# Performance work log

Hardware: AMD Instinct MI355X
Metric: run time of the kernel (lower is better)

## Reference

```python
import jax, jax.numpy as jnp
import numpy as np

H, DH = 16, 64            # heads, dim_head
SCALE = DH ** -0.5
TOPK = 32                  # sparse_topk


def setup_inputs() -> dict:
    key = jax.random.key(0)
    ks = jax.random.split(key, 8)
    b, n, dim = 2, 1024, 1024
    inner = H * DH
    x = jax.random.normal(ks[0], (b, n, dim), jnp.float32)
    rel_pos = jax.random.normal(ks[1], (1, H, n, n), jnp.float32)
    Wq = jax.random.normal(ks[2], (dim, inner), jnp.float32) * 0.02
    Wkv = jax.random.normal(ks[3], (dim, 2 * inner), jnp.float32) * 0.02
    pre_proj = jax.random.normal(ks[4], (H, H), jnp.float32)   # pre_softmax_proj
    post_proj = jax.random.normal(ks[5], (H, H), jnp.float32)  # post_softmax_proj
    Wout = jax.random.normal(ks[6], (inner, dim), jnp.float32) * 0.02
    bout = jnp.zeros((dim,), jnp.float32)
    return dict(x=x, rel_pos=rel_pos, Wq=Wq, Wkv=Wkv, pre_proj=pre_proj,
                post_proj=post_proj, Wout=Wout, bout=bout)


def reference(x, rel_pos, Wq, Wkv, pre_proj, post_proj, Wout, bout):
    b, n, _ = x.shape
    # projections (no bias, matching nn.Linear(..., bias=False))
    q = (x @ Wq).reshape(b, n, H, DH).transpose(0, 2, 1, 3)          # b h n d
    k, v = jnp.split(x @ Wkv, 2, axis=-1)
    k = k.reshape(b, n, H, DH).transpose(0, 2, 1, 3)
    v = v.reshape(b, n, H, DH).transpose(0, 2, 1, 3)
    # scores + rel_pos bias
    dots = jnp.einsum('bhid,bhjd->bhij', q, k) * SCALE + rel_pos
    # talking heads (pre-softmax), applied BEFORE masks as in the source
    dots = jnp.einsum('bhij,hk->bkij', dots, pre_proj)
    neg = -jnp.finfo(dots.dtype).max
    # causal mask
    causal = jnp.triu(jnp.ones((n, n), dtype=bool), 1)
    dots = jnp.where(causal, neg, dots)
    # sparse top-k masking: keep only entries >= k-th largest per row
    kth = jax.lax.top_k(dots, TOPK)[0][..., -1:]
    dots = jnp.where(dots < kth, neg, dots)
    attn = jax.nn.softmax(dots, axis=-1)
    # talking heads (post-softmax)
    attn = jnp.einsum('bhij,hk->bkij', attn, post_proj)
    out = jnp.einsum('bhij,bhjd->bhid', attn, v)
    out = out.transpose(0, 2, 1, 3).reshape(b, n, H * DH)
    return out @ Wout + bout
```

## Files before the change

### kernel.cpp

```cpp
#include <hip/hip_runtime.h>
#include <hip/hip_bf16.h>
#include <float.h>
#include <math.h>

#define HH 16
#define DH 64
#define NS 1024
#define SCALE 0.125f
#define KTOP 32
#define NEGF (-FLT_MAX)

typedef __attribute__((ext_vector_type(8))) short short8;
typedef __attribute__((ext_vector_type(4))) float f32x4;
typedef unsigned short ushort_t;

__device__ __forceinline__ ushort_t f2b(float f) {
    __hip_bfloat16 h = __float2bfloat16(f);
    return *reinterpret_cast<ushort_t*>(&h);
}

__global__ __launch_bounds__(256) void k0_cvt(const float* __restrict__ src,
        ushort_t* __restrict__ dst, int n8) {
    int i = blockIdx.x * 256 + threadIdx.x;
    if (i >= n8) return;
    const float4* s4 = (const float4*)src;
    float4 a = s4[i*2], b = s4[i*2+1];
    short8 o;
    o[0]=f2b(a.x); o[1]=f2b(a.y); o[2]=f2b(a.z); o[3]=f2b(a.w);
    o[4]=f2b(b.x); o[5]=f2b(b.y); o[6]=f2b(b.z); o[7]=f2b(b.w);
    *(short8*)(dst + i*8) = o;
}

__global__ __launch_bounds__(256) void k0_tr(const float* __restrict__ src,
        ushort_t* __restrict__ dst, int N) {
    __shared__ float sh[32][33];
    int tx = threadIdx.x & 31, ty = threadIdx.x >> 5;
    int n0 = blockIdx.x * 32, k0 = blockIdx.y * 32;
    #pragma unroll
    for (int e = 0; e < 4; ++e) {
        int r = ty + e*8;
        sh[r][tx] = src[(k0 + r)*N + n0 + tx];
    }
    __syncthreads();
    #pragma unroll
    for (int e = 0; e < 4; ++e) {
        int r = ty + e*8;
        dst[(n0 + r)*1024 + k0 + tx] = f2b(sh[tx][r]);
    }
}

__global__ __launch_bounds__(256) void k1_mfma(const ushort_t* __restrict__ xb,
        const ushort_t* __restrict__ Wt, ushort_t* __restrict__ qb,
        ushort_t* __restrict__ kbf, ushort_t* __restrict__ vb) {
    __shared__ ushort_t As[128*40];
    __shared__ ushort_t Bs[128*40];
    int t = threadIdx.x;
    int lane = t & 63, w = t >> 6;
    int wm = w >> 1, wn = w & 1;
    int row_l = lane & 15, grp = lane >> 4;
    int row0 = blockIdx.y * 128, col0 = blockIdx.x * 128;
    f32x4 acc[4][4];
    f32x4 zz = {0.f, 0.f, 0.f, 0.f};
    #pragma unroll
    for (int mi = 0; mi < 4; ++mi)
        #pragma unroll
        for (int ni = 0; ni < 4; ++ni) acc[mi][ni] = zz;
    for (int k0 = 0; k0 < 1024; k0 += 32) {
        #pragma unroll
        for (int e = 0; e < 2; ++e) {
            int slot = t + 256*e;
            int r = slot >> 2, kbk = slot & 3;
            short8 vA = *(const short8*)(xb + (row0 + r)*1024 + k0 + kbk*8);
            *(short8*)(As + r*40 + kbk*8) = vA;
            short8 vB = *(const short8*)(Wt + (col0 + r)*1024 + k0 + kbk*8);
            *(short8*)(Bs + r*40 + kbk*8) = vB;
        }
        __syncthreads();
        short8 a[4], b[4];
        #pragma unroll
        for (int mi = 0; mi < 4; ++mi)
            a[mi] = *(const short8*)(As + (wm*64 + mi*16 + row_l)*40 + grp*8);
        #pragma unroll
        for (int ni = 0; ni < 4; ++ni)
            b[ni] = *(const short8*)(Bs + (wn*64 + ni*16 + row_l)*40 + grp*8);
        #pragma unroll
        for (int mi = 0; mi < 4; ++mi)
            #pragma unroll
            for (int ni = 0; ni < 4; ++ni)
                acc[mi][ni] = __builtin_amdgcn_mfma_f32_16x16x32_bf16(
                    a[mi], b[ni], acc[mi][ni], 0, 0, 0);
        __syncthreads();
    }
    #pragma unroll
    for (int mi = 0; mi < 4; ++mi)
        #pragma unroll
        for (int ni = 0; ni < 4; ++ni)
            #pragma unroll
            for (int rg = 0; rg < 4; ++rg) {
                int grow = row0 + wm*64 + mi*16 + grp*4 + rg;
                int gcol = col0 + wn*64 + ni*16 + row_l;
                float val = acc[mi][ni][rg];
                int b_ = grow >> 10, i = grow & 1023;
                int which = gcol >> 10, cc = gcol & 1023;
                int h = cc >> 6, d = cc & 63;
                int idx = (((b_*HH + h)*NS) + i)*DH + d;
                if (which == 0)      qb[idx]  = f2b(val);
                else if (which == 1) kbf[idx] = f2b(val);
                else                 vb[idx]  = f2b(val);
            }
}

__global__ __launch_bounds__(256) void k4_vt(const ushort_t* __restrict__ vb,
        ushort_t* __restrict__ vT) {
    __shared__ ushort_t sh[32][33];
    int bh = blockIdx.z;
    int d0 = blockIdx.x * 32;
    int i0 = blockIdx.y * 32;
    int tx = threadIdx.x & 31, ty = threadIdx.x >> 5;
    #pragma unroll
    for (int e = 0; e < 4; ++e) {
        int r = ty + e*8;
        sh[r][tx] = vb[((size_t)bh*NS + i0 + r)*DH + d0 + tx];
    }
    __syncthreads();
    #pragma unroll
    for (int e = 0; e < 4; ++e) {
        int r = ty + e*8;
        vT[((size_t)bh*DH + d0 + r)*NS + i0 + tx] = sh[tx][r];
    }
}

__global__ __launch_bounds__(256) void k2_scores(const ushort_t* __restrict__ qb,
        const ushort_t* __restrict__ kbf, const float* __restrict__ rel,
        const float* __restrict__ pre, float* __restrict__ dots) {
    int t = threadIdx.x & 63;
    int w = threadIdx.x >> 6;
    int wid = blockIdx.x * 4 + w;
    int b_ = (wid >= 2080) ? 1 : 0;
    int r = wid - 2080*b_;
    int i16 = (int)((sqrtf(8.0f*(float)r + 1.0f) - 1.0f) * 0.5f);
    while ((i16+1)*(i16+2)/2 <= r) ++i16;
    while (i16*(i16+1)/2 > r) --i16;
    int j16 = r - i16*(i16+1)/2;
    int row_l = t & 15, grp = t >> 4;
    int qrow = i16*16 + row_l;
    int krow = j16*16 + row_l;
    int dbase = grp*8;
    float acc[16][4];
    #pragma unroll
    for (int kp = 0; kp < 16; ++kp)
        #pragma unroll
        for (int rg = 0; rg < 4; ++rg) acc[kp][rg] = 0.f;
    #pragma unroll 4
    for (int h = 0; h < HH; ++h) {
        const ushort_t* qh = qb + (((b_*HH + h)*NS) + qrow)*DH;
        const ushort_t* kh = kbf + (((b_*HH + h)*NS) + krow)*DH;
        short8 a0 = *(const short8*)(qh + dbase);
        short8 a1 = *(const short8*)(qh + 32 + dbase);
        short8 b0 = *(const short8*)(kh + dbase);
        short8 b1 = *(const short8*)(kh + 32 + dbase);
        f32x4 s = {0.f, 0.f, 0.f, 0.f};
        s = __builtin_amdgcn_mfma_f32_16x16x32_bf16(a0, b0, s, 0, 0, 0);
        s = __builtin_amdgcn_mfma_f32_16x16x32_bf16(a1, b1, s, 0, 0, 0);
        float pr[16];
        #pragma unroll
        for (int kp = 0; kp < 16; ++kp) pr[kp] = pre[h*16 + kp];
        #pragma unroll
        for (int rg = 0; rg < 4; ++rg) {
            int gi = i16*16 + grp*4 + rg;
            int gj = j16*16 + row_l;
            float tv = s[rg]*SCALE + rel[(h*NS + gi)*NS + gj];
            #pragma unroll
            for (int kp = 0; kp < 16; ++kp) acc[kp][rg] += tv * pr[kp];
        }
    }
    int gj = j16*16 + row_l;
    #pragma unroll
    for (int kp = 0; kp < 16; ++kp)
        #pragma unroll
        for (int rg = 0; rg < 4; ++rg) {
            int gi = i16*16 + grp*4 + rg;
            dots[(((b_*HH + kp)*NS) + gi)*NS + gj] = acc[kp][rg];
        }
}

template<int NC>
__device__ __forceinline__ void topk_row(const float* __restrict__ rowp,
        float* __restrict__ scRow, int i, int l) {
    float v[NC*4];
    unsigned u[NC*4];
    #pragma unroll
    for (int c = 0; c < NC; ++c) {
        float4 t4 = *(const float4*)(rowp + c*256 + l*4);
        v[c*4+0] = t4.x; v[c*4+1] = t4.y; v[c*4+2] = t4.z; v[c*4+3] = t4.w;
    }
    #pragma unroll
    for (int c = 0; c < NC; ++c) {
        int j0 = c*256 + l*4;
        #pragma unroll
        for (int e = 0; e < 4; ++e)
            if (j0 + e > i) v[c*4+e] = NEGF;
    }
    float m = NEGF;
    #pragma unroll
    for (int e = 0; e < NC*4; ++e) m = fmaxf(m, v[e]);
    #pragma unroll
    for (int o = 32; o; o >>= 1) m = fmaxf(m, __shfl_xor(m, o));
    #pragma unroll
    for (int e = 0; e < NC*4; ++e) {
        unsigned x = __float_as_uint(v[e]);
        u[e] = x ^ ((unsigned)(((int)x) >> 31) | 0x80000000u);
    }
    unsigned thr = 0u;
    for (int bit = 31; bit >= 0; --bit) {
        unsigned cand = thr | (1u << bit);
        int cnt = 0;
        #pragma unroll
        for (int e = 0; e < NC*4; ++e)
            cnt += __popcll(__ballot(u[e] >= cand));
        if (cnt >= KTOP) thr = cand;
    }
    float ssum = 0.f;
    #pragma unroll
    for (int e = 0; e < NC*4; ++e) {
        float ev = (u[e] >= thr) ? __expf(v[e] - m) : 0.f;
        v[e] = ev; ssum += ev;
    }
    #pragma unroll
    for (int o = 32; o; o >>= 1) ssum += __shfl_xor(ssum, o);
    float inv = 1.0f / ssum;
    #pragma unroll
    for (int c = 0; c < NC; ++c) {
        float4 o4;
        o4.x = v[c*4+0] * inv; o4.y = v[c*4+1] * inv;
        o4.z = v[c*4+2] * inv; o4.w = v[c*4+3] * inv;
        *(float4*)(scRow + c*256 + l*4) = o4;
    }
    float4 z4 = {0.f, 0.f, 0.f, 0.f};
    #pragma unroll
    for (int c = NC; c < 4; ++c)
        *(float4*)(scRow + c*256 + l*4) = z4;
}

__global__ __launch_bounds__(1024, 4) void k3_topk(float* __restrict__ dots,
        const float* __restrict__ post) {
    __shared__ float sc[HH][NS];
    __shared__ float postS[HH][HH];
    int t = threadIdx.x;
    int bi = blockIdx.x;
    int b_ = bi >> 10, i = bi & 1023;
    if (t < 256) postS[t >> 4][t & 15] = post[t];
    int w = t >> 6;
    int l = t & 63;
    const float* rowp = dots + ((size_t)((b_*HH + w)*NS + i))*NS;
    int nc = (i >> 8) + 1;
    if (nc == 1)      topk_row<1>(rowp, sc[w], i, l);
    else if (nc == 2) topk_row<2>(rowp, sc[w], i, l);
    else if (nc == 3) topk_row<3>(rowp, sc[w], i, l);
    else              topk_row<4>(rowp, sc[w], i, l);
    __syncthreads();
    ushort_t* pb = (ushort_t*)dots;
    float a16[HH];
    #pragma unroll
    for (int h = 0; h < HH; ++h) a16[h] = sc[h][t];
    #pragma unroll
    for (int kp = 0; kp < HH; ++kp) {
        float o = 0.f;
        #pragma unroll
        for (int h = 0; h < HH; ++h) o += a16[h] * postS[h][kp];
        pb[(((size_t)(b_*HH + kp)*NS + i)*NS << 1) + t] = f2b(o);
    }
}

__global__ __launch_bounds__(256) void k5_pv(const ushort_t* __restrict__ pb,
        const ushort_t* __restrict__ vT, ushort_t* __restrict__ ao) {
    int t = threadIdx.x;
    int lane = t & 63, w = t >> 6;
    int bh = blockIdx.y;
    int i0 = blockIdx.x * 64;
    int row_l = lane & 15, grp = lane >> 4;
    int irow = i0 + w*16 + row_l;
    const ushort_t* pA = pb + (((size_t)bh*NS + irow)*NS << 1);
    const ushort_t* vB = vT + ((size_t)bh*DH + row_l)*NS;
    f32x4 acc[4];
    f32x4 zz = {0.f, 0.f, 0.f, 0.f};
    #pragma unroll
    for (int ni = 0; ni < 4; ++ni) acc[ni] = zz;
    int nsteps = (i0 + 64) >> 5;
    for (int s = 0; s < nsteps; ++s) {
        int j0 = s*32 + grp*8;
        short8 a = *(const short8*)(pA + j0);
        #pragma unroll
        for (int ni = 0; ni < 4; ++ni) {
            short8 b = *(const short8*)(vB + ni*16*NS + j0);
            acc[ni] = __builtin_amdgcn_mfma_f32_16x16x32_bf16(a, b, acc[ni], 0, 0, 0);
        }
    }
    #pragma unroll
    for (int ni = 0; ni < 4; ++ni)
        #pragma unroll
        for (int rg = 0; rg < 4; ++rg)
            ao[((size_t)bh*NS + i0 + w*16 + grp*4 + rg)*DH + ni*16 + row_l] = f2b(acc[ni][rg]);
}

__global__ __launch_bounds__(256) void k6_mfma(const ushort_t* __restrict__ aob,
        const ushort_t* __restrict__ Wot, const float* __restrict__ bout,
        float* __restrict__ y) {
    __shared__ ushort_t As[128*40];
    __shared__ ushort_t Bs[128*40];
    int t = threadIdx.x;
    int lane = t & 63, w = t >> 6;
    int wm = w >> 1, wn = w & 1;
    int row_l = lane & 15, grp = lane >> 4;
    int row0 = blockIdx.y * 128, col0 = blockIdx.x * 128;
    f32x4 acc[4][4];
    f32x4 zz = {0.f, 0.f, 0.f, 0.f};
    #pragma unroll
    for (int mi = 0; mi < 4; ++mi)
        #pragma unroll
        for (int ni = 0; ni < 4; ++ni) acc[mi][ni] = zz;
    for (int k0 = 0; k0 < 1024; k0 += 32) {
        #pragma unroll
        for (int e = 0; e < 2; ++e) {
            int slot = t + 256*e;
            int r = slot >> 2, kbk = slot & 3;
            int grow = row0 + r;
            int b_ = grow >> 10, i = grow & 1023;
            int kk0 = k0 + kbk*8;
            int h = kk0 >> 6, d = kk0 & 63;
            short8 vA = *(const short8*)(aob + (((b_*HH + h)*NS) + i)*DH + d);
            *(short8*)(As + r*40 + kbk*8) = vA;
            short8 vB = *(const short8*)(Wot + (col0 + r)*1024 + k0 + kbk*8);
            *(short8*)(Bs + r*40 + kbk*8) = vB;
        }
        __syncthreads();
        short8 a[4], b[4];
        #pragma unroll
        for (int mi = 0; mi < 4; ++mi)
            a[mi] = *(const short8*)(As + (wm*64 + mi*16 + row_l)*40 + grp*8);
        #pragma unroll
        for (int ni = 0; ni < 4; ++ni)
            b[ni] = *(const short8*)(Bs + (wn*64 + ni*16 + row_l)*40 + grp*8);
        #pragma unroll
        for (int mi = 0; mi < 4; ++mi)
            #pragma unroll
            for (int ni = 0; ni < 4; ++ni)
                acc[mi][ni] = __builtin_amdgcn_mfma_f32_16x16x32_bf16(
                    a[mi], b[ni], acc[mi][ni], 0, 0, 0);
        __syncthreads();
    }
    #pragma unroll
    for (int mi = 0; mi < 4; ++mi)
        #pragma unroll
        for (int ni = 0; ni < 4; ++ni)
            #pragma unroll
            for (int rg = 0; rg < 4; ++rg) {
                int grow = row0 + wm*64 + mi*16 + grp*4 + rg;
                int gcol = col0 + wn*64 + ni*16 + row_l;
                y[grow*1024 + gcol] = acc[mi][ni][rg] + bout[gcol];
            }
}

extern "C" void kernel_launch(void* const* d_in, const int* in_sizes, int n_in,
                              void* d_out, int out_size, void* d_ws, size_t ws_size,
                              hipStream_t stream) {
    const float* x    = (const float*)d_in[0];
    const float* rel  = (const float*)d_in[1];
    const float* Wq   = (const float*)d_in[2];
    const float* Wkv  = (const float*)d_in[3];
    const float* pre  = (const float*)d_in[4];
    const float* post = (const float*)d_in[5];
    const float* Wout = (const float*)d_in[6];
    const float* bout = (const float*)d_in[7];
    float* out = (float*)d_out;

    float* ws = (float*)d_ws;
    float*    dots = ws;
    ushort_t* vb   = (ushort_t*)(ws + 33554432);
    ushort_t* vT   = (ushort_t*)(ws + 34603008);
    ushort_t* qb   = (ushort_t*)(ws + 35651584);
    ushort_t* kbuf = (ushort_t*)(ws + 36700160);
    ushort_t* xb   = (ushort_t*)(ws + 37748736);
    ushort_t* Wt   = (ushort_t*)(ws + 38797312);
    ushort_t* Wot  = (ushort_t*)(ws + 40370176);
    ushort_t* aob  = (ushort_t*)(ws + 40894464);

    k0_cvt<<<1024, 256, 0, stream>>>(x, xb, 262144);
    k0_tr<<<dim3(32, 32), 256, 0, stream>>>(Wq, Wt, 1024);
    k0_tr<<<dim3(64, 32), 256, 0, stream>>>(Wkv, Wt + 1024*1024, 2048);
    k0_tr<<<dim3(32, 32), 256, 0, stream>>>(Wout, Wot, 1024);
    k1_mfma<<<dim3(24, 16), 256, 0, stream>>>(xb, Wt, qb, kbuf, vb);
    k4_vt<<<dim3(2, 32, 32), 256, 0, stream>>>(vb, vT);
    k2_scores<<<dim3(1040), 256, 0, stream>>>(qb, kbuf, rel, pre, dots);
    k3_topk<<<dim3(2048), 1024, 0, stream>>>(dots, post);
    k5_pv<<<dim3(16, 32), 256, 0, stream>>>((const ushort_t*)dots, vT, aob);
    k6_mfma<<<dim3(8, 16), 256, 0, stream>>>(aob, Wot, bout, out);
}
```

Baseline: 340.4 us.

## Fuse x conversion into QKV GEMM, shrink top-k smem to bf16, shorten radix search

```diff
diff --git a/kernel.cpp b/kernel.cpp
--- a/kernel.cpp
+++ b/kernel.cpp
@@ -11,6 +11,7 @@
 #define NEGF (-FLT_MAX)
 
 typedef __attribute__((ext_vector_type(8))) short short8;
+typedef __attribute__((ext_vector_type(4))) short short4v;
 typedef __attribute__((ext_vector_type(4))) float f32x4;
 typedef unsigned short ushort_t;
 
@@ -18,17 +19,9 @@
     __hip_bfloat16 h = __float2bfloat16(f);
     return *reinterpret_cast<ushort_t*>(&h);
 }
-
-__global__ __launch_bounds__(256) void k0_cvt(const float* __restrict__ src,
-        ushort_t* __restrict__ dst, int n8) {
-    int i = blockIdx.x * 256 + threadIdx.x;
-    if (i >= n8) return;
-    const float4* s4 = (const float4*)src;
-    float4 a = s4[i*2], b = s4[i*2+1];
-    short8 o;
-    o[0]=f2b(a.x); o[1]=f2b(a.y); o[2]=f2b(a.z); o[3]=f2b(a.w);
-    o[4]=f2b(b.x); o[5]=f2b(b.y); o[6]=f2b(b.z); o[7]=f2b(b.w);
-    *(short8*)(dst + i*8) = o;
+__device__ __forceinline__ float b2f(ushort_t u) {
+    unsigned x = ((unsigned)u) << 16;
+    return __uint_as_float(x);
 }
 
 __global__ __launch_bounds__(256) void k0_tr(const float* __restrict__ src,
@@ -49,7 +42,7 @@
     }
 }
 
-__global__ __launch_bounds__(256) void k1_mfma(const ushort_t* __restrict__ xb,
+__global__ __launch_bounds__(256) void k1_mfma(const float* __restrict__ xf,
         const ushort_t* __restrict__ Wt, ushort_t* __restrict__ qb,
         ushort_t* __restrict__ kbf, ushort_t* __restrict__ vb) {
     __shared__ ushort_t As[128*40];
@@ -70,9 +63,14 @@
         for (int e = 0; e < 2; ++e) {
             int slot = t + 256*e;
             int r = slot >> 2, kbk = slot & 3;
-            short8 vA = *(const short8*)(xb + (row0 + r)*1024 + k0 + kbk*8);
+            const float* xs = xf + (size_t)(row0 + r)*1024 + k0 + kbk*8;
+            float4 xa = *(const float4*)(xs);
+            float4 xbv = *(const float4*)(xs + 4);
+            short8 vA;
+            vA[0]=f2b(xa.x); vA[1]=f2b(xa.y); vA[2]=f2b(xa.z); vA[3]=f2b(xa.w);
+            vA[4]=f2b(xbv.x); vA[5]=f2b(xbv.y); vA[6]=f2b(xbv.z); vA[7]=f2b(xbv.w);
             *(short8*)(As + r*40 + kbk*8) = vA;
-            short8 vB = *(const short8*)(Wt + (col0 + r)*1024 + k0 + kbk*8);
+            short8 vB = *(const short8*)(Wt + (size_t)(col0 + r)*1024 + k0 + kbk*8);
             *(short8*)(Bs + r*40 + kbk*8) = vB;
         }
         __syncthreads();
@@ -186,7 +184,7 @@
 
 template<int NC>
 __device__ __forceinline__ void topk_row(const float* __restrict__ rowp,
-        float* __restrict__ scRow, int i, int l) {
+        ushort_t* __restrict__ scRow, int i, int l) {
     float v[NC*4];
     unsigned u[NC*4];
     #pragma unroll
@@ -212,7 +210,7 @@
         u[e] = x ^ ((unsigned)(((int)x) >> 31) | 0x80000000u);
     }
     unsigned thr = 0u;
-    for (int bit = 31; bit >= 0; --bit) {
+    for (int bit = 31; bit >= 8; --bit) {
         unsigned cand = thr | (1u << bit);
         int cnt = 0;
         #pragma unroll
@@ -231,20 +229,22 @@
     float inv = 1.0f / ssum;
     #pragma unroll
     for (int c = 0; c < NC; ++c) {
-        float4 o4;
-        o4.x = v[c*4+0] * inv; o4.y = v[c*4+1] * inv;
-        o4.z = v[c*4+2] * inv; o4.w = v[c*4+3] * inv;
-        *(float4*)(scRow + c*256 + l*4) = o4;
-    }
-    float4 z4 = {0.f, 0.f, 0.f, 0.f};
+        short4v o4;
+        o4[0] = (short)f2b(v[c*4+0] * inv);
+        o4[1] = (short)f2b(v[c*4+1] * inv);
+        o4[2] = (short)f2b(v[c*4+2] * inv);
+        o4[3] = (short)f2b(v[c*4+3] * inv);
+        *(short4v*)(scRow + c*256 + l*4) = o4;
+    }
+    short4v z4 = {0, 0, 0, 0};
     #pragma unroll
     for (int c = NC; c < 4; ++c)
-        *(float4*)(scRow + c*256 + l*4) = z4;
+        *(short4v*)(scRow + c*256 + l*4) = z4;
 }
 
 __global__ __launch_bounds__(1024, 4) void k3_topk(float* __restrict__ dots,
         const float* __restrict__ post) {
-    __shared__ float sc[HH][NS];
+    __shared__ ushort_t sc[HH][NS];
     __shared__ float postS[HH][HH];
     int t = threadIdx.x;
     int bi = blockIdx.x;
@@ -262,7 +262,7 @@
     ushort_t* pb = (ushort_t*)dots;
     float a16[HH];
     #pragma unroll
-    for (int h = 0; h < HH; ++h) a16[h] = sc[h][t];
+    for (int h = 0; h < HH; ++h) a16[h] = b2f(sc[h][t]);
     #pragma unroll
     for (int kp = 0; kp < HH; ++kp) {
         float o = 0.f;
@@ -330,7 +330,7 @@
             int h = kk0 >> 6, d = kk0 & 63;
             short8 vA = *(const short8*)(aob + (((b_*HH + h)*NS) + i)*DH + d);
             *(short8*)(As + r*40 + kbk*8) = vA;
-            short8 vB = *(const short8*)(Wot + (col0 + r)*1024 + k0 + kbk*8);
+            short8 vB = *(const short8*)(Wot + (size_t)(col0 + r)*1024 + k0 + kbk*8);
             *(short8*)(Bs + r*40 + kbk*8) = vB;
         }
         __syncthreads();
@@ -380,16 +380,14 @@
     ushort_t* vT   = (ushort_t*)(ws + 34603008);
     ushort_t* qb   = (ushort_t*)(ws + 35651584);
     ushort_t* kbuf = (ushort_t*)(ws + 36700160);
-    ushort_t* xb   = (ushort_t*)(ws + 37748736);
     ushort_t* Wt   = (ushort_t*)(ws + 38797312);
     ushort_t* Wot  = (ushort_t*)(ws + 40370176);
     ushort_t* aob  = (ushort_t*)(ws + 40894464);
 
-    k0_cvt<<<1024, 256, 0, stream>>>(x, xb, 262144);
     k0_tr<<<dim3(32, 32), 256, 0, stream>>>(Wq, Wt, 1024);
     k0_tr<<<dim3(64, 32), 256, 0, stream>>>(Wkv, Wt + 1024*1024, 2048);
     k0_tr<<<dim3(32, 32), 256, 0, stream>>>(Wout, Wot, 1024);
-    k1_mfma<<<dim3(24, 16), 256, 0, stream>>>(xb, Wt, qb, kbuf, vb);
+    k1_mfma<<<dim3(24, 16), 256, 0, stream>>>(x, Wt, qb, kbuf, vb);
     k4_vt<<<dim3(2, 32, 32), 256, 0, stream>>>(vb, vT);
     k2_scores<<<dim3(1040), 256, 0, stream>>>(qb, kbuf, rel, pre, dots);
     k3_topk<<<dim3(2048), 1024, 0, stream>>>(dots, post);
```

After: 368.5 us. +8.3%, slower.
